# Kernel optimization log

Hardware: AMD Instinct MI355X
Metric: run time of the kernel (lower is better)

The kernel has to match this reference:

```python
import jax, jax.numpy as jnp
import numpy as np

EPS = 1e-8
B, T, D = 2, 512, 64
L = 4        # n_layers
NPASS = 2    # n_recursive_passes


def setup_inputs() -> dict:
    key = jax.random.key(0)
    ks = jax.random.split(key, 8)
    H = D // 2
    r = lambda k, shape, s=0.05: jax.random.normal(k, shape, dtype=jnp.float32) * s
    return {
        "basin_seq": jax.random.normal(ks[0], (B, T, D), dtype=jnp.float32),
        "basin_coords": r(ks[1], (D,), 0.1),
        "W_temp": r(ks[2], (L, 1, D)),
        "b_temp": jnp.zeros((L, 1), jnp.float32),
        "res_scale": jnp.full((L,), 0.1, jnp.float32),
        "W_fb": r(ks[3], (L, D, 2 * D)),
        "b_fb": jnp.zeros((L, D), jnp.float32),
        "Wc1": r(ks[4], (H, D)),
        "bc1": jnp.zeros((H,), jnp.float32),
        "Wc2": r(ks[5], (D, H)),
        "bc2": jnp.zeros((D,), jnp.float32),
        "Wu": r(ks[6], (D, 2 * D)),
        "bu": jnp.zeros((D,), jnp.float32),
        "res_scale_g": jnp.asarray(1.0, jnp.float32),
    }


def _project_to_simplex(x):
    s = jax.nn.softplus(x)
    s = s / (s.sum(axis=-1, keepdims=True) + EPS)
    return jnp.maximum(s, EPS)


def _qfi_attention_weights(x, temperature):
    # x: (B,T,D); temperature: scalar
    p = _project_to_simplex(x)
    # fisher_rao_distance_simplex renormalizes its inputs again
    p = p / (p.sum(axis=-1, keepdims=True) + EPS)
    # pairwise Bhattacharyya-like inner product: (B,T,T,D) broadcast -> (B,T,T)
    inner = jnp.sqrt(p[:, :, None, :] * p[:, None, :, :] + EPS).sum(axis=-1)
    inner = jnp.clip(inner, -1.0 + 1e-6, 1.0 - 1e-6)
    d = 2.0 * jnp.arccos(inner)                      # Fisher-Rao distance (B,T,T)
    logits = -d / jnp.maximum(temperature, 1e-6)
    return jax.nn.softmax(logits, axis=-1)


def _forward(basin_seq, basin_coords, W_temp, b_temp, res_scale, W_fb, b_fb,
             Wc1, bc1, Wc2, bc2, Wu, bu, res_scale_g):
    x = basin_seq
    current_basin = basin_coords                     # (D,)
    layer_states = [[None] * L for _ in range(NPASS)]
    for p_idx in range(NPASS):
        for l in range(L):
            prev = layer_states[p_idx - 1][l] if p_idx > 0 else None
            if prev is not None:
                combined = jnp.concatenate([x, prev], axis=-1)          # (B,T,2D)
                gate = jax.nn.sigmoid(combined @ W_fb[l].T + b_fb[l])   # (B,T,D)
                x = x * gate + prev * (1.0 - gate)
            # BasinCoupledQFIAttention (dropout inactive in eval)
            tm = jax.nn.sigmoid(W_temp[l] @ current_basin + b_temp[l]) + 0.5
            temperature = jax.lax.stop_gradient(tm.mean())  # torch uses .item()
            w = _qfi_attention_weights(x, temperature)
            x_attn = jnp.einsum('bij,bjd->bid', w, x)
            x = x + res_scale[l] * (x_attn - x)
            layer_states[p_idx][l] = x
        # holographic encode: mean-pool then compress MLP (tanh, tanh)
        pooled = x.mean(axis=1)                                         # (B,D)
        hidden_basin = jnp.tanh(jnp.tanh(pooled @ Wc1.T + bc1) @ Wc2.T + bc2)
        if p_idx < NPASS - 1:
            aggregated = hidden_basin.mean(axis=0)                      # (D,)
            comb = jnp.concatenate([current_basin, aggregated], axis=-1)
            g = jax.nn.sigmoid(Wu @ comb + bu)
            current_basin = current_basin * (1.0 - g) + aggregated * g
    output = x + 0.01 * res_scale_g * (x - basin_seq)
    return output


def reference(basin_seq, basin_coords, W_temp, b_temp, res_scale, W_fb, b_fb,
              Wc1, bc1, Wc2, bc2, Wu, bu, res_scale_g):
    return _forward(basin_seq, basin_coords, W_temp, b_temp, res_scale, W_fb,
                    b_fb, Wc1, bc1, Wc2, bc2, Wu, bu, res_scale_g)
```

## Files before the change

kernel.cpp:

```cpp
#include <hip/hip_runtime.h>
#include <math.h>

#define EPSF 1e-8f
#define Tn 512
#define Dn 64
#define NELEM 65536

typedef _Float16 half_t;
typedef __attribute__((ext_vector_type(8))) _Float16 half8;

__device__ __forceinline__ float sigmoidf_(float x){ return 1.0f/(1.0f+__expf(-x)); }
__device__ __forceinline__ float softplusf_(float x){ return fmaxf(x,0.0f) + log1pf(__expf(-fabsf(x))); }

__device__ __forceinline__ float wrs(float v){
  #pragma unroll
  for (int off=1; off<64; off<<=1) v += __shfl_xor(v, off, 64);
  return v;
}
__device__ __forceinline__ float wrm(float v){
  #pragma unroll
  for (int off=1; off<64; off<<=1) v = fmaxf(v, __shfl_xor(v, off, 64));
  return v;
}

__device__ __forceinline__ void pnorm_h(float xg, int b, int r, int lane,
                                        half_t* __restrict__ sTh){
  float s = softplusf_(xg);
  float sum = wrs(s);
  float p = fmaxf(s/(sum+EPSF), EPSF);
  float s2 = wrs(p);
  float sq = sqrtf(p/(s2+EPSF));
  float v[8];
  #pragma unroll
  for (int m=0;m<8;m++) v[m] = __shfl(sq, (lane&7)*8 + m, 64);
  if (lane < 8){
    half8 hv;
    #pragma unroll
    for (int m=0;m<8;m++) hv[m] = (half_t)v[m];
    ((half8*)sTh)[((size_t)b*8 + lane)*512 + r] = hv;
  }
}

__device__ __forceinline__ void gate_dot2(float (*comb)[128], float* gred,
                                          const float* __restrict__ Wfb, int tid, int lane){
  int dd = tid >> 3, k8 = tid & 7;
  const float4* wp = (const float4*)(Wfb + (size_t)dd*128 + k8*16);
  float4 w0 = wp[0], w1 = wp[1], w2 = wp[2], w3 = wp[3];
  float ga[2];
  #pragma unroll
  for (int i=0;i<2;i++){
    float4 c0 = *(const float4*)&comb[i][k8*16];
    float4 c1 = *(const float4*)&comb[i][k8*16+4];
    float4 c2 = *(const float4*)&comb[i][k8*16+8];
    float4 c3 = *(const float4*)&comb[i][k8*16+12];
    ga[i] = w0.x*c0.x + w0.y*c0.y + w0.z*c0.z + w0.w*c0.w
          + w1.x*c1.x + w1.y*c1.y + w1.z*c1.z + w1.w*c1.w
          + w2.x*c2.x + w2.y*c2.y + w2.z*c2.z + w2.w*c2.w
          + w3.x*c3.x + w3.y*c3.y + w3.z*c3.z + w3.w*c3.w;
  }
  #pragma unroll
  for (int off=1; off<8; off<<=1){
    ga[0] += __shfl_xor(ga[0],off,64); ga[1] += __shfl_xor(ga[1],off,64);
  }
  if ((lane&7)==0){ gred[dd*3+0]=ga[0]; gred[dd*3+1]=ga[1]; }
}

__global__ __launch_bounds__(256) void k_prologue(
    const float* __restrict__ basin_seq, half_t* __restrict__ sThA,
    half_t* __restrict__ h_bs,
    const float* __restrict__ W_temp, const float* __restrict__ b_temp,
    const float* __restrict__ cb0, float* __restrict__ temps0, float* __restrict__ pooled_g){
  int tid = threadIdx.x, wid = tid>>6, lane = tid&63;
  if (blockIdx.x < 256){
    int row = blockIdx.x*4 + wid;
    float xv = basin_seq[(size_t)row*Dn + lane];
    h_bs[(size_t)row*Dn + lane] = (half_t)xv;
    pnorm_h(xv, row>>9, row&511, lane, sThA);
  } else {
    if (tid < 64){
      float cbv = cb0[tid];
      #pragma unroll
      for (int l=0;l<4;l++){
        float v = wrs(W_temp[l*Dn + tid]*cbv);
        if (tid==0) temps0[l] = sigmoidf_(v + b_temp[l]) + 0.5f;
      }
    }
    if (tid < 128) pooled_g[tid] = 0.f;
  }
}

template<int MODE>
__global__ __launch_bounds__(512) void k_attn(
    const half_t* __restrict__ xh_in, const half_t* __restrict__ sTh_in,
    const float* __restrict__ temps_in, const float* __restrict__ res_scale, int l,
    half_t* __restrict__ xh_out, half_t* __restrict__ sTh_out,
    const float* __restrict__ Wfb, const float* __restrict__ bfb,
    const half_t* __restrict__ prevh,
    half_t* __restrict__ h3out, float* __restrict__ pooled_g, float* __restrict__ temps_out,
    const float* __restrict__ basin_coords,
    const float* __restrict__ Wc1, const float* __restrict__ bc1,
    const float* __restrict__ Wc2, const float* __restrict__ bc2,
    const float* __restrict__ Wu, const float* __restrict__ bu,
    const float* __restrict__ W_temp, const float* __restrict__ b_temp,
    const float* __restrict__ basin_seq, const float* __restrict__ rsg,
    float* __restrict__ out_f){

  __shared__ __align__(16) float pvp[128*64];
  __shared__ __align__(16) float P[512*2];
  __shared__ __align__(16) float s01[128];
  __shared__ float redw[2][8][2];
  __shared__ __align__(16) float comb[2][128];
  __shared__ float gred[192];
  __shared__ float temps_l[4];
  __shared__ float pooled_l[128];
  __shared__ float h1l[64];
  __shared__ float hbl[128];
  __shared__ float combb[128];
  __shared__ float nb_l[64];

  int tid = threadIdx.x, wav = tid>>6, lane = tid&63;
  int row0 = blockIdx.x*2, b = row0>>9, rb = row0&511;
  int i_ = tid>>6, d_ = lane;

  if constexpr (MODE == 2){
    if (tid < 128) pooled_l[tid] = pooled_g[tid];
    __syncthreads();
    if (tid < 64){
      int bb = tid>>5, h = tid&31;
      float acc=0.f;
      #pragma unroll 8
      for (int d2=0; d2<64; d2++) acc += pooled_l[bb*64+d2]*Wc1[h*64+d2];
      h1l[tid] = tanhf(acc + bc1[h]);
    }
    __syncthreads();
    if (tid < 128){
      int bb = tid>>6, d = tid&63;
      float acc=0.f;
      #pragma unroll 8
      for (int h2=0; h2<32; h2++) acc += h1l[bb*32+h2]*Wc2[d*32+h2];
      hbl[tid] = tanhf(acc + bc2[d]);
    }
    __syncthreads();
    if (tid < 64){
      combb[tid] = basin_coords[tid];
      combb[64+tid] = 0.5f*(hbl[tid] + hbl[64+tid]);
    }
    __syncthreads();
    if (tid < 64){
      float acc=0.f;
      #pragma unroll 8
      for (int k=0;k<128;k++) acc += Wu[tid*128+k]*combb[k];
      float g = sigmoidf_(acc + bu[tid]);
      nb_l[tid] = combb[tid]*(1.0f-g) + combb[64+tid]*g;
    }
    __syncthreads();
    if (tid < 64){
      float nb = nb_l[tid];
      #pragma unroll
      for (int l2=0;l2<4;l2++){
        float v = wrs(W_temp[l2*Dn + tid]*nb);
        if (tid==0) temps_l[l2] = sigmoidf_(v + b_temp[l2]) + 0.5f;
      }
    }
    __syncthreads();
    if (tid < 4) temps_out[tid] = temps_l[tid];
  }

  float xi_pre = 0.f, prev_pre = 0.f;
  if (tid < 128){
    half8 hv = ((const half8*)sTh_in)[((size_t)b*8 + (d_>>3))*512 + (rb+i_)];
    s01[d_*2 + i_] = (float)hv[d_&7];
    xi_pre = (float)xh_in[(size_t)(row0+i_)*Dn + d_];
    if constexpr (MODE == 1 || MODE == 2 || MODE == 3)
      prev_pre = (float)prevh[(size_t)(row0+i_)*Dn + d_];
  }
  __syncthreads();

  float invT;
  if constexpr (MODE == 2) invT = 1.0f/fmaxf(temps_l[0], 1e-6f);
  else                     invT = 1.0f/fmaxf(temps_in[l], 1e-6f);

  float a0=0.f, a1=0.f;
  {
    const half8* sT8 = (const half8*)sTh_in + (size_t)b*8*512;
    const float4* sp = (const float4*)s01;
    #pragma unroll
    for (int c8=0;c8<8;++c8){
      half8 kv = sT8[(size_t)c8*512 + tid];
      float kf[8];
      #pragma unroll
      for (int m=0;m<8;m++) kf[m] = (float)kv[m];
      #pragma unroll
      for (int q=0;q<4;q++){
        float4 sv = sp[c8*4+q];
        a0 = fmaf(kf[2*q],   sv.x, a0); a1 = fmaf(kf[2*q],   sv.y, a1);
        a0 = fmaf(kf[2*q+1], sv.z, a0); a1 = fmaf(kf[2*q+1], sv.w, a1);
      }
    }
  }
  {
    float c0 = fminf(fmaxf(a0,-1.0f+1e-6f),1.0f-1e-6f);
    float c1 = fminf(fmaxf(a1,-1.0f+1e-6f),1.0f-1e-6f);
    float l0 = -2.0f*acosf(c0)*invT;
    float l1 = -2.0f*acosf(c1)*invT;
    float m0=wrm(l0), m1=wrm(l1);
    if (lane==0){ redw[0][wav][0]=m0; redw[0][wav][1]=m1; }
    __syncthreads();
    float mv0=redw[0][0][0], mv1=redw[0][0][1];
    #pragma unroll
    for (int w=1;w<8;w++){ mv0=fmaxf(mv0,redw[0][w][0]); mv1=fmaxf(mv1,redw[0][w][1]); }
    float e0=__expf(l0-mv0), e1=__expf(l1-mv1);
    *(float2*)&P[tid*2] = make_float2(e0,e1);
    float q0=wrs(e0), q1=wrs(e1);
    if (lane==0){ redw[1][wav][0]=q0; redw[1][wav][1]=q1; }
  }
  __syncthreads();
  {
    int jg = tid>>3, dq8 = tid&7;
    const half8* x8 = (const half8*)(xh_in + (size_t)b*Tn*Dn);
    float o0[8], o1[8];
    #pragma unroll
    for (int m=0;m<8;m++){ o0[m]=0.f; o1[m]=0.f; }
    #pragma unroll
    for (int jj=0; jj<8; ++jj){
      int j = jj*64 + jg;
      half8 xv = x8[(size_t)j*8 + dq8];
      float2 pw = *(const float2*)&P[j*2];
      #pragma unroll
      for (int m=0;m<8;m++){
        float xf = (float)xv[m];
        o0[m] = fmaf(pw.x, xf, o0[m]);
        o1[m] = fmaf(pw.y, xf, o1[m]);
      }
    }
    float* p0 = &pvp[(jg*2+0)*64 + dq8*8];
    float* p1 = &pvp[(jg*2+1)*64 + dq8*8];
    *(float4*)p0     = make_float4(o0[0],o0[1],o0[2],o0[3]);
    *(float4*)(p0+4) = make_float4(o0[4],o0[5],o0[6],o0[7]);
    *(float4*)p1     = make_float4(o1[0],o1[1],o1[2],o1[3]);
    *(float4*)(p1+4) = make_float4(o1[4],o1[5],o1[6],o1[7]);
  }
  __syncthreads();
  float o = 0.f;
  if (tid < 128){
    float ss = 0.f;
    #pragma unroll
    for (int g=0; g<64; ++g) ss += pvp[(g*2+i_)*64+d_];
    float sv = 0.f;
    #pragma unroll
    for (int w=0;w<8;w++) sv += redw[1][w][i_];
    o = xi_pre + res_scale[l]*(ss/sv - xi_pre);
  }

  if constexpr (MODE == 0){
    if (tid < 128){
      xh_out[(size_t)(row0+i_)*Dn + d_] = (half_t)o;
      pnorm_h(o, b, rb+i_, lane, sTh_out);
    }
  } else if constexpr (MODE == 4){
    if (tid < 128){
      float c = 0.01f * rsg[0];
      out_f[(size_t)(row0+i_)*Dn + d_] = o + c*(o - basin_seq[(size_t)(row0+i_)*Dn + d_]);
    }
  } else {
    if (tid < 128){
      if constexpr (MODE == 1) h3out[(size_t)(row0+i_)*Dn + d_] = (half_t)o;
      comb[i_][d_] = o;
      comb[i_][64+d_] = prev_pre;
    }
    __syncthreads();
    if constexpr (MODE == 1){
      if (tid < 64)
        atomicAdd(&pooled_g[b*Dn + tid], (comb[0][tid]+comb[1][tid]) * (1.0f/Tn));
    }
    gate_dot2(comb, gred, Wfb, tid, lane);
    __syncthreads();
    if (tid < 128){
      float g = sigmoidf_(gred[d_*3+i_] + bfb[d_]);
      float xg = o*g + prev_pre*(1.0f-g);
      xh_out[(size_t)(row0+i_)*Dn + d_] = (half_t)xg;
      pnorm_h(xg, b, rb+i_, lane, sTh_out);
    }
  }
}

extern "C" void kernel_launch(void* const* d_in, const int* in_sizes, int n_in,
                              void* d_out, int out_size, void* d_ws, size_t ws_size,
                              hipStream_t stream) {
  const float* basin_seq    = (const float*)d_in[0];
  const float* basin_coords = (const float*)d_in[1];
  const float* W_temp       = (const float*)d_in[2];
  const float* b_temp       = (const float*)d_in[3];
  const float* res_scale    = (const float*)d_in[4];
  const float* W_fb         = (const float*)d_in[5];
  const float* b_fb         = (const float*)d_in[6];
  const float* Wc1          = (const float*)d_in[7];
  const float* bc1          = (const float*)d_in[8];
  const float* Wc2          = (const float*)d_in[9];
  const float* bc2          = (const float*)d_in[10];
  const float* Wu           = (const float*)d_in[11];
  const float* bu           = (const float*)d_in[12];
  const float* rsg          = (const float*)d_in[13];
  float* out = (float*)d_out;
  float* ws  = (float*)d_ws;

  const size_t N = NELEM;
  float* pooled   = ws;
  float* temps0   = ws + 128;
  float* temps_p1 = ws + 136;
  half_t* hb   = (half_t*)(ws + 256);
  half_t* h_bs = hb + 0*N;
  half_t* h0   = hb + 1*N;
  half_t* h1   = hb + 2*N;
  half_t* h2   = hb + 3*N;
  half_t* h3   = hb + 4*N;
  half_t* hA   = hb + 5*N;
  half_t* hB   = hb + 6*N;
  half_t* sThA = hb + 7*N;
  half_t* sThB = hb + 8*N;

  const int GA = 512;
  const size_t WFB = (size_t)Dn*2*Dn;

  k_prologue<<<257,256,0,stream>>>(basin_seq, sThA, h_bs,
                                   W_temp, b_temp, basin_coords, temps0, pooled);
  k_attn<0><<<GA,512,0,stream>>>(h_bs, sThA, temps0, res_scale, 0,
      h0, sThB, nullptr,nullptr,nullptr, nullptr,nullptr,nullptr,
      nullptr,nullptr,nullptr,nullptr,nullptr,nullptr,nullptr,nullptr,nullptr,nullptr,nullptr,nullptr);
  k_attn<0><<<GA,512,0,stream>>>(h0, sThB, temps0, res_scale, 1,
      h1, sThA, nullptr,nullptr,nullptr, nullptr,nullptr,nullptr,
      nullptr,nullptr,nullptr,nullptr,nullptr,nullptr,nullptr,nullptr,nullptr,nullptr,nullptr,nullptr);
  k_attn<0><<<GA,512,0,stream>>>(h1, sThA, temps0, res_scale, 2,
      h2, sThB, nullptr,nullptr,nullptr, nullptr,nullptr,nullptr,
      nullptr,nullptr,nullptr,nullptr,nullptr,nullptr,nullptr,nullptr,nullptr,nullptr,nullptr,nullptr);
  k_attn<1><<<GA,512,0,stream>>>(h2, sThB, temps0, res_scale, 3,
      hA, sThA, W_fb, b_fb, h0, h3, pooled, nullptr,
      nullptr,nullptr,nullptr,nullptr,nullptr,nullptr,nullptr,nullptr,nullptr,nullptr,nullptr,nullptr);
  k_attn<2><<<GA,512,0,stream>>>(hA, sThA, nullptr, res_scale, 0,
      hB, sThB, W_fb + 1*WFB, b_fb + 1*Dn, h1, nullptr, pooled, temps_p1,
      basin_coords, Wc1, bc1, Wc2, bc2, Wu, bu, W_temp, b_temp, nullptr,nullptr,nullptr);
  k_attn<3><<<GA,512,0,stream>>>(hB, sThB, temps_p1, res_scale, 1,
      hA, sThA, W_fb + 2*WFB, b_fb + 2*Dn, h2, nullptr,nullptr,nullptr,
      nullptr,nullptr,nullptr,nullptr,nullptr,nullptr,nullptr,nullptr,nullptr,nullptr,nullptr,nullptr);
  k_attn<3><<<GA,512,0,stream>>>(hA, sThA, temps_p1, res_scale, 2,
      hB, sThB, W_fb + 3*WFB, b_fb + 3*Dn, h3, nullptr,nullptr,nullptr,
      nullptr,nullptr,nullptr,nullptr,nullptr,nullptr,nullptr,nullptr,nullptr,nullptr,nullptr,nullptr);
  k_attn<4><<<GA,512,0,stream>>>(hB, sThB, temps_p1, res_scale, 3,
      nullptr, nullptr, nullptr,nullptr,nullptr, nullptr,nullptr,nullptr,
      nullptr,nullptr,nullptr,nullptr,nullptr,nullptr,nullptr,nullptr,nullptr,
      basin_seq, rsg, out);
}
```

Before: 169.0 us.

## Fuse prologue into first attention layer, recomputing simplex projection per key row

Removes the separate prologue kernel. A new first-layer kernel reads fp32 basin_seq directly, recomputes the softplus/simplex projection of every key row inside each block, and computes the temperatures and pooled zeroing itself. This saves one launch and the half-precision staging buffers, and layer 0 now runs in fp32. In exchange every block redundantly projects all 512 key rows of its batch, which costs extra transcendental work.

```diff
diff --git a/kernel.cpp b/kernel.cpp
--- a/kernel.cpp
+++ b/kernel.cpp
@@ -11,6 +11,7 @@
 
 __device__ __forceinline__ float sigmoidf_(float x){ return 1.0f/(1.0f+__expf(-x)); }
 __device__ __forceinline__ float softplusf_(float x){ return fmaxf(x,0.0f) + log1pf(__expf(-fabsf(x))); }
+__device__ __forceinline__ float softplus_fast(float x){ return fmaxf(x,0.0f) + __logf(1.0f+__expf(-fabsf(x))); }
 
 __device__ __forceinline__ float wrs(float v){
   #pragma unroll
@@ -65,27 +66,130 @@
   if ((lane&7)==0){ gred[dd*3+0]=ga[0]; gred[dd*3+1]=ga[1]; }
 }
 
-__global__ __launch_bounds__(256) void k_prologue(
-    const float* __restrict__ basin_seq, half_t* __restrict__ sThA,
-    half_t* __restrict__ h_bs,
+__global__ __launch_bounds__(512) void k_attn0(
+    const float* __restrict__ basin_seq, const float* __restrict__ basin_coords,
     const float* __restrict__ W_temp, const float* __restrict__ b_temp,
-    const float* __restrict__ cb0, float* __restrict__ temps0, float* __restrict__ pooled_g){
-  int tid = threadIdx.x, wid = tid>>6, lane = tid&63;
-  if (blockIdx.x < 256){
-    int row = blockIdx.x*4 + wid;
-    float xv = basin_seq[(size_t)row*Dn + lane];
-    h_bs[(size_t)row*Dn + lane] = (half_t)xv;
-    pnorm_h(xv, row>>9, row&511, lane, sThA);
-  } else {
-    if (tid < 64){
-      float cbv = cb0[tid];
-      #pragma unroll
-      for (int l=0;l<4;l++){
-        float v = wrs(W_temp[l*Dn + tid]*cbv);
-        if (tid==0) temps0[l] = sigmoidf_(v + b_temp[l]) + 0.5f;
-      }
-    }
-    if (tid < 128) pooled_g[tid] = 0.f;
+    const float* __restrict__ res_scale,
+    half_t* __restrict__ xh_out, half_t* __restrict__ sTh_out,
+    float* __restrict__ temps_out, float* __restrict__ pooled_g){
+
+  __shared__ __align__(16) float pvp[64*64];
+  __shared__ __align__(16) float P[512*2];
+  __shared__ __align__(16) float s01[128];
+  __shared__ float redw[2][8][2];
+  __shared__ float temps_l[4];
+
+  int tid = threadIdx.x, wav = tid>>6, lane = tid&63;
+  int row0 = blockIdx.x*2, b = row0>>9, rb = row0&511;
+  int i_ = tid>>6, d_ = lane;
+
+  if (tid < 64){
+    float cbv = basin_coords[tid];
+    #pragma unroll
+    for (int l2=0;l2<4;l2++){
+      float v = wrs(W_temp[l2*Dn + tid]*cbv);
+      if (tid==0) temps_l[l2] = sigmoidf_(v + b_temp[l2]) + 0.5f;
+    }
+  }
+  if (blockIdx.x==0 && tid<128) pooled_g[tid] = 0.f;
+
+  float xi_pre = 0.f;
+  if (tid < 128){
+    float xv = basin_seq[(size_t)(row0+i_)*Dn + d_];
+    xi_pre = xv;
+    float s = softplusf_(xv);
+    float sum = wrs(s);
+    float p = fmaxf(s/(sum+EPSF), EPSF);
+    float s2 = wrs(p);
+    s01[d_*2 + i_] = sqrtf(p/(s2+EPSF));
+  }
+  __syncthreads();
+  if (blockIdx.x==0 && tid<4) temps_out[tid] = temps_l[tid];
+
+  float invT = 1.0f/fmaxf(temps_l[0], 1e-6f);
+
+  float a0=0.f, a1=0.f;
+  {
+    const float4* rowp = (const float4*)(basin_seq + (size_t)b*Tn*Dn + (size_t)tid*Dn);
+    float sv[64];
+    float t0=0.f,t1=0.f,t2=0.f,t3=0.f;
+    #pragma unroll
+    for (int c=0;c<16;c++){
+      float4 x4 = rowp[c];
+      sv[4*c+0]=softplus_fast(x4.x); sv[4*c+1]=softplus_fast(x4.y);
+      sv[4*c+2]=softplus_fast(x4.z); sv[4*c+3]=softplus_fast(x4.w);
+      t0+=sv[4*c+0]; t1+=sv[4*c+1]; t2+=sv[4*c+2]; t3+=sv[4*c+3];
+    }
+    float inv1 = 1.0f/((t0+t1+t2+t3)+EPSF);
+    t0=t1=t2=t3=0.f;
+    #pragma unroll
+    for (int c=0;c<16;c++){
+      sv[4*c+0]=fmaxf(sv[4*c+0]*inv1, EPSF); t0+=sv[4*c+0];
+      sv[4*c+1]=fmaxf(sv[4*c+1]*inv1, EPSF); t1+=sv[4*c+1];
+      sv[4*c+2]=fmaxf(sv[4*c+2]*inv1, EPSF); t2+=sv[4*c+2];
+      sv[4*c+3]=fmaxf(sv[4*c+3]*inv1, EPSF); t3+=sv[4*c+3];
+    }
+    float inv2 = 1.0f/((t0+t1+t2+t3)+EPSF);
+    const float4* sp = (const float4*)s01;
+    #pragma unroll
+    for (int c=0;c<16;c++){
+      float q0 = sqrtf(sv[4*c+0]*inv2);
+      float q1 = sqrtf(sv[4*c+1]*inv2);
+      float q2 = sqrtf(sv[4*c+2]*inv2);
+      float q3 = sqrtf(sv[4*c+3]*inv2);
+      float4 sA = sp[2*c], sB = sp[2*c+1];
+      a0=fmaf(q0,sA.x,a0); a1=fmaf(q0,sA.y,a1);
+      a0=fmaf(q1,sA.z,a0); a1=fmaf(q1,sA.w,a1);
+      a0=fmaf(q2,sB.x,a0); a1=fmaf(q2,sB.y,a1);
+      a0=fmaf(q3,sB.z,a0); a1=fmaf(q3,sB.w,a1);
+    }
+  }
+  {
+    float c0 = fminf(fmaxf(a0,-1.0f+1e-6f),1.0f-1e-6f);
+    float c1 = fminf(fmaxf(a1,-1.0f+1e-6f),1.0f-1e-6f);
+    float l0 = -2.0f*acosf(c0)*invT;
+    float l1 = -2.0f*acosf(c1)*invT;
+    float m0=wrm(l0), m1=wrm(l1);
+    if (lane==0){ redw[0][wav][0]=m0; redw[0][wav][1]=m1; }
+    __syncthreads();
+    float mv0=redw[0][0][0], mv1=redw[0][0][1];
+    #pragma unroll
+    for (int w=1;w<8;w++){ mv0=fmaxf(mv0,redw[0][w][0]); mv1=fmaxf(mv1,redw[0][w][1]); }
+    float e0=__expf(l0-mv0), e1=__expf(l1-mv1);
+    *(float2*)&P[tid*2] = make_float2(e0,e1);
+    float q0=wrs(e0), q1=wrs(e1);
+    if (lane==0){ redw[1][wav][0]=q0; redw[1][wav][1]=q1; }
+  }
+  __syncthreads();
+  {
+    int jg = tid>>4, dq = tid&15;
+    const float4* x4p = (const float4*)(basin_seq + (size_t)b*Tn*Dn);
+    float4 o0={0,0,0,0}, o1={0,0,0,0};
+    int jb = jg*16;
+    #pragma unroll 8
+    for (int jj=0; jj<16; ++jj){
+      int j = jb + jj;
+      float4 xv = x4p[(size_t)j*16 + dq];
+      float2 pw = *(const float2*)&P[j*2];
+      o0.x=fmaf(pw.x,xv.x,o0.x); o0.y=fmaf(pw.x,xv.y,o0.y);
+      o0.z=fmaf(pw.x,xv.z,o0.z); o0.w=fmaf(pw.x,xv.w,o0.w);
+      o1.x=fmaf(pw.y,xv.x,o1.x); o1.y=fmaf(pw.y,xv.y,o1.y);
+      o1.z=fmaf(pw.y,xv.z,o1.z); o1.w=fmaf(pw.y,xv.w,o1.w);
+    }
+    *(float4*)&pvp[(jg*2+0)*64 + dq*4] = o0;
+    *(float4*)&pvp[(jg*2+1)*64 + dq*4] = o1;
+  }
+  __syncthreads();
+  if (tid < 128){
+    float ss = 0.f;
+    #pragma unroll
+    for (int g=0; g<32; ++g) ss += pvp[(g*2+i_)*64+d_];
+    float sv2 = 0.f;
+    #pragma unroll
+    for (int w=0;w<8;w++) sv2 += redw[1][w][i_];
+    float o = xi_pre + res_scale[0]*(ss/sv2 - xi_pre);
+    xh_out[(size_t)(row0+i_)*Dn + d_] = (half_t)o;
+    pnorm_h(o, b, rb+i_, lane, sTh_out);
   }
 }
 
@@ -309,43 +413,39 @@
   float* temps0   = ws + 128;
   float* temps_p1 = ws + 136;
   half_t* hb   = (half_t*)(ws + 256);
-  half_t* h_bs = hb + 0*N;
-  half_t* h0   = hb + 1*N;
-  half_t* h1   = hb + 2*N;
-  half_t* h2   = hb + 3*N;
-  half_t* h3   = hb + 4*N;
-  half_t* hA   = hb + 5*N;
-  half_t* hB   = hb + 6*N;
-  half_t* sThA = hb + 7*N;
-  half_t* sThB = hb + 8*N;
+  half_t* h0   = hb + 0*N;
+  half_t* h1   = hb + 1*N;
+  half_t* h2   = hb + 2*N;
+  half_t* h3   = hb + 3*N;
+  half_t* hA   = hb + 4*N;
+  half_t* hB   = hb + 5*N;
+  half_t* sThA = hb + 6*N;
+  half_t* sThB = hb + 7*N;
 
   const int GA = 512;
   const size_t WFB = (size_t)Dn*2*Dn;
 
-  k_prologue<<<257,256,0,stream>>>(basin_seq, sThA, h_bs,
-                                   W_temp, b_temp, basin_coords, temps0, pooled);
-  k_attn<0><<<GA,512,0,stream>>>(h_bs, sThA, temps0, res_scale, 0,
-      h0, sThB, nullptr,nullptr,nullptr, nullptr,nullptr,nullptr,
+  k_attn0<<<GA,512,0,stream>>>(basin_seq, basin_coords, W_temp, b_temp, res_scale,
+                               h0, sThA, temps0, pooled);
+  k_attn<0><<<GA,512,0,stream>>>(h0, sThA, temps0, res_scale, 1,
+      h1, sThB, nullptr,nullptr,nullptr, nullptr,nullptr,nullptr,
       nullptr,nullptr,nullptr,nullptr,nullptr,nullptr,nullptr,nullptr,nullptr,nullptr,nullptr,nullptr);
-  k_attn<0><<<GA,512,0,stream>>>(h0, sThB, temps0, res_scale, 1,
-      h1, sThA, nullptr,nullptr,nullptr, nullptr,nullptr,nullptr,
+  k_attn<0><<<GA,512,0,stream>>>(h1, sThB, temps0, res_scale, 2,
+      h2, sThA, nullptr,nullptr,nullptr, nullptr,nullptr,nullptr,
       nullptr,nullptr,nullptr,nullptr,nullptr,nullptr,nullptr,nullptr,nullptr,nullptr,nullptr,nullptr);
-  k_attn<0><<<GA,512,0,stream>>>(h1, sThA, temps0, res_scale, 2,
-      h2, sThB, nullptr,nullptr,nullptr, nullptr,nullptr,nullptr,
+  k_attn<1><<<GA,512,0,stream>>>(h2, sThA, temps0, res_scale, 3,
+      hA, sThB, W_fb, b_fb, h0, h3, pooled, nullptr,
       nullptr,nullptr,nullptr,nullptr,nullptr,nullptr,nullptr,nullptr,nullptr,nullptr,nullptr,nullptr);
-  k_attn<1><<<GA,512,0,stream>>>(h2, sThB, temps0, res_scale, 3,
-      hA, sThA, W_fb, b_fb, h0, h3, pooled, nullptr,
+  k_attn<2><<<GA,512,0,stream>>>(hA, sThB, nullptr, res_scale, 0,
+      hB, sThA, W_fb + 1*WFB, b_fb + 1*Dn, h1, nullptr, pooled, temps_p1,
+      basin_coords, Wc1, bc1, Wc2, bc2, Wu, bu, W_temp, b_temp, nullptr,nullptr,nullptr);
+  k_attn<3><<<GA,512,0,stream>>>(hB, sThA, temps_p1, res_scale, 1,
+      hA, sThB, W_fb + 2*WFB, b_fb + 2*Dn, h2, nullptr,nullptr,nullptr,
       nullptr,nullptr,nullptr,nullptr,nullptr,nullptr,nullptr,nullptr,nullptr,nullptr,nullptr,nullptr);
-  k_attn<2><<<GA,512,0,stream>>>(hA, sThA, nullptr, res_scale, 0,
-      hB, sThB, W_fb + 1*WFB, b_fb + 1*Dn, h1, nullptr, pooled, temps_p1,
-      basin_coords, Wc1, bc1, Wc2, bc2, Wu, bu, W_temp, b_temp, nullptr,nullptr,nullptr);
-  k_attn<3><<<GA,512,0,stream>>>(hB, sThB, temps_p1, res_scale, 1,
-      hA, sThA, W_fb + 2*WFB, b_fb + 2*Dn, h2, nullptr,nullptr,nullptr,
+  k_attn<3><<<GA,512,0,stream>>>(hA, sThB, temps_p1, res_scale, 2,
+      hB, sThA, W_fb + 3*WFB, b_fb + 3*Dn, h3, nullptr,nullptr,nullptr,
       nullptr,nullptr,nullptr,nullptr,nullptr,nullptr,nullptr,nullptr,nullptr,nullptr,nullptr,nullptr);
-  k_attn<3><<<GA,512,0,stream>>>(hA, sThA, temps_p1, res_scale, 2,
-      hB, sThB, W_fb + 3*WFB, b_fb + 3*Dn, h3, nullptr,nullptr,nullptr,
-      nullptr,nullptr,nullptr,nullptr,nullptr,nullptr,nullptr,nullptr,nullptr,nullptr,nullptr,nullptr);
-  k_attn<4><<<GA,512,0,stream>>>(hB, sThB, temps_p1, res_scale, 3,
+  k_attn<4><<<GA,512,0,stream>>>(hB, sThA, temps_p1, res_scale, 3,
       nullptr, nullptr, nullptr,nullptr,nullptr, nullptr,nullptr,nullptr,
       nullptr,nullptr,nullptr,nullptr,nullptr,nullptr,nullptr,nullptr,nullptr,
       basin_seq, rsg, out);
```

After: 182.4 us. 1.08x slower.
